# Kernel optimization log

Hardware: AMD Instinct MI355X
Metric: run time of the kernel (lower is better)

## Reference

```python
import jax, jax.numpy as jnp
import numpy as np

LAYERS = 3
EMB = 256
B = 4096
N_ITEMS = 50000
MAX_LEN = 50
EPS = 1e-12  # F.normalize eps


def setup_inputs() -> dict:
    key = jax.random.key(0)
    k1, k2, k3, k4, k5, k6 = jax.random.split(key, 6)
    item_embedding = jax.random.normal(k1, (N_ITEMS, EMB), dtype=jnp.float32)
    D = jax.random.uniform(k2, (B, B), dtype=jnp.float32)
    A = jax.random.uniform(k3, (B, B), dtype=jnp.float32)
    # indices into padded table of size N_ITEMS+1 (row 0 is the zero pad row)
    session_item = jax.random.randint(k4, (B, MAX_LEN), 0, N_ITEMS + 1, dtype=jnp.int64)
    session_len = jax.random.randint(k5, (B, 1), 1, MAX_LEN + 1).astype(jnp.float32)
    w_sess = jax.random.normal(k6, (LAYERS, EMB, EMB), dtype=jnp.float32) * (1.0 / np.sqrt(EMB))
    return {"item_embedding": item_embedding, "D": D, "A": A,
            "session_item": session_item, "session_len": session_len,
            "w_sess": w_sess}


def reference(item_embedding, D, A, session_item, session_len, w_sess):
    # prepend zero pad row, then gather: [B, L, E]
    emb = jnp.concatenate([jnp.zeros((1, item_embedding.shape[1]), item_embedding.dtype),
                           item_embedding], axis=0)
    seq_h = emb[session_item]                      # fused gather (no host round-trip)
    session_emb = seq_h.sum(axis=1) / session_len  # [B, E] mean pooling

    DA = D @ A                                     # [B, B]
    acc = session_emb                              # layer-0 (unnormalized) term
    x = session_emb
    for i in range(LAYERS):
        x = x @ w_sess[i].T                        # torch Linear: y = x W^T
        x = DA @ x                                 # dense GCN propagation
        norm = jnp.maximum(jnp.linalg.norm(x, axis=-1, keepdims=True), EPS)
        acc = acc + x / norm                       # normalized copy stored; x stays raw
    return acc / (LAYERS + 1)
```

## Files before the change

kernel.cpp:

```cpp
#include <hip/hip_runtime.h>
#include <hip/hip_bf16.h>
#include <cstdint>
#include <cstddef>

#define LAYERS 3
#define EMB 256
#define NB 4096
#define MAXLEN 50
#define NITEMS 50000

typedef float f32x4 __attribute__((ext_vector_type(4)));
typedef __bf16 bf16x8 __attribute__((ext_vector_type(8)));
typedef unsigned short u16;
typedef __attribute__((ext_vector_type(8))) unsigned short u16x8;

static __device__ __forceinline__ u16 f2bf(float f) {
  union { float f; uint32_t u; } v; v.f = f;
  uint32_t r = v.u + 0x7FFFu + ((v.u >> 16) & 1u);
  return (u16)(r >> 16);
}

static __device__ __forceinline__ float bf2f(u16 h) {
  union { uint32_t u; float f; } v; v.u = (uint32_t)h << 16; return v.f;
}

static __device__ __forceinline__ f32x4 bfu4(ushort4 h) {
  f32x4 r; r.x = bf2f(h.x); r.y = bf2f(h.y); r.z = bf2f(h.z); r.w = bf2f(h.w);
  return r;
}

static __device__ __forceinline__ ushort4 f2bf4(f32x4 v) {
  ushort4 o; o.x = f2bf(v.x); o.y = f2bf(v.y); o.z = f2bf(v.z); o.w = f2bf(v.w);
  return o;
}

template <typename T> __device__ __forceinline__ T cvt_out(float v);
template <> __device__ __forceinline__ float cvt_out<float>(float v) { return v; }
template <> __device__ __forceinline__ u16 cvt_out<u16>(float v) { return f2bf(v); }

#define N8_D (NB * NB / 8)
#define N8_W (LAYERS * EMB * EMB / 8)
#define N8_E ((NITEMS + 1) * EMB / 8)

__global__ void pack_all(const float* __restrict__ D, const float* __restrict__ A,
                         const float* __restrict__ w, const float* __restrict__ emb,
                         u16* __restrict__ Db, u16* __restrict__ Ab,
                         u16* __restrict__ wb, u16* __restrict__ ebp) {
  const int total = N8_D + N8_D + N8_W + N8_E;
  for (int i = blockIdx.x * blockDim.x + threadIdx.x; i < total;
       i += gridDim.x * blockDim.x) {
    int j = i;
    const float* src; u16* dst;
    if (j < N8_D) {
      src = D + (size_t)j * 8; dst = Db + (size_t)j * 8;
    } else if ((j -= N8_D) < N8_D) {
      src = A + (size_t)j * 8; dst = Ab + (size_t)j * 8;
    } else if ((j -= N8_D) < N8_W) {
      src = w + (size_t)j * 8; dst = wb + (size_t)j * 8;
    } else {
      j -= N8_W;
      dst = ebp + (size_t)j * 8;
      if (j < EMB / 8) {
        u16x8 z = {0, 0, 0, 0, 0, 0, 0, 0};
        *reinterpret_cast<u16x8*>(dst) = z;
        continue;
      }
      src = emb + (size_t)(j - EMB / 8) * 8;
    }
    f32x4 lo = *reinterpret_cast<const f32x4*>(src);
    f32x4 hi = *reinterpret_cast<const f32x4*>(src + 4);
    ushort4 a = f2bf4(lo), b = f2bf4(hi);
    u16x8 o = {a.x, a.y, a.z, a.w, b.x, b.y, b.z, b.w};
    *reinterpret_cast<u16x8*>(dst) = o;
  }
}

__global__ void gather_mean(const u16* __restrict__ ebp, const int* __restrict__ items,
                            const float* __restrict__ slen, float* __restrict__ acc,
                            u16* __restrict__ xb) {
  int w = threadIdx.x >> 6, lane = threadIdx.x & 63;
  int b = blockIdx.x * 4 + w;
  f32x4 s = {0.f, 0.f, 0.f, 0.f};
  const int* it = items + (size_t)b * MAXLEN;
  const int le = lane * 4;
#pragma unroll 2
  for (int l = 0; l < MAXLEN; l += 5) {
    int i0 = it[l], i1 = it[l + 1], i2 = it[l + 2], i3 = it[l + 3], i4 = it[l + 4];
    ushort4 v0 = *reinterpret_cast<const ushort4*>(ebp + (size_t)i0 * EMB + le);
    ushort4 v1 = *reinterpret_cast<const ushort4*>(ebp + (size_t)i1 * EMB + le);
    ushort4 v2 = *reinterpret_cast<const ushort4*>(ebp + (size_t)i2 * EMB + le);
    ushort4 v3 = *reinterpret_cast<const ushort4*>(ebp + (size_t)i3 * EMB + le);
    ushort4 v4 = *reinterpret_cast<const ushort4*>(ebp + (size_t)i4 * EMB + le);
    s += bfu4(v0) + bfu4(v1) + bfu4(v2) + bfu4(v3) + bfu4(v4);
  }
  float inv = 1.0f / slen[b];
  s *= inv;
  *reinterpret_cast<f32x4*>(acc + (size_t)b * EMB + le) = s;
  *reinterpret_cast<ushort4*>(xb + (size_t)b * EMB + le) = f2bf4(s);
}

template <int WR, int WC, typename OUT_T>
__global__ __launch_bounds__(512, 4) void gemm_w(const u16* __restrict__ Am,
                                                 const u16* __restrict__ Bt,
                                                 OUT_T* __restrict__ C,
                                                 int M, int N, int K, size_t zstride) {
  constexpr int TM = WR * 64, TN = WC * 64;
  __shared__ __align__(16) u16 As[TM * 64];
  __shared__ __align__(16) u16 Bs[TN * 64];
  const int tid = threadIdx.x;
  const int lane = tid & 63;
  const int wid = tid >> 6;
  const int wm = wid / WC, wn = wid % WC;
  const int row0 = blockIdx.y * TM, col0 = blockIdx.x * TN;
  const int kslice = K / (int)gridDim.z;
  const int kb = blockIdx.z * kslice, ke = kb + kslice;
  C += (size_t)blockIdx.z * zstride;

  f32x4 acc[4][4];
#pragma unroll
  for (int m = 0; m < 4; m++)
#pragma unroll
    for (int n = 0; n < 4; n++)
#pragma unroll
      for (int j = 0; j < 4; j++) acc[m][n][j] = 0.0f;

  const int lrow = lane & 15;
  const int lhi = lane >> 4;
  const int sw7 = lane & 7;
  const int srow = tid >> 3;
  const int schk = tid & 7;

  for (int k0 = kb; k0 < ke; k0 += 64) {
#pragma unroll
    for (int i = 0; i < WR; i++) {
      int row = i * 64 + srow;
      int sc = schk ^ (row & 7);
      __builtin_amdgcn_global_load_lds(
          (const __attribute__((address_space(1))) void*)(Am + (size_t)(row0 + row) * K + k0 + sc * 8),
          (__attribute__((address_space(3))) void*)(As + (size_t)(i * 512 + tid) * 8), 16, 0, 0);
    }
#pragma unroll
    for (int i = 0; i < WC; i++) {
      int row = i * 64 + srow;
      int sc = schk ^ (row & 7);
      __builtin_amdgcn_global_load_lds(
          (const __attribute__((address_space(1))) void*)(Bt + (size_t)(col0 + row) * K + k0 + sc * 8),
          (__attribute__((address_space(3))) void*)(Bs + (size_t)(i * 512 + tid) * 8), 16, 0, 0);
    }
    __syncthreads();

#pragma unroll
    for (int kk = 0; kk < 2; kk++) {
      const int co = ((kk * 4 + lhi) ^ sw7) * 8;
      bf16x8 af[4], bfv[4];
#pragma unroll
      for (int m = 0; m < 4; m++)
        af[m] = *reinterpret_cast<const bf16x8*>(As + (size_t)(wm * 64 + m * 16 + lrow) * 64 + co);
#pragma unroll
      for (int n = 0; n < 4; n++)
        bfv[n] = *reinterpret_cast<const bf16x8*>(Bs + (size_t)(wn * 64 + n * 16 + lrow) * 64 + co);
#pragma unroll
      for (int m = 0; m < 4; m++)
#pragma unroll
        for (int n = 0; n < 4; n++)
          acc[m][n] = __builtin_amdgcn_mfma_f32_16x16x32_bf16(af[m], bfv[n], acc[m][n], 0, 0, 0);
    }
    __syncthreads();
  }

#pragma unroll
  for (int m = 0; m < 4; m++) {
#pragma unroll
    for (int j = 0; j < 4; j++) {
      int r = row0 + wm * 64 + m * 16 + lhi * 4 + j;
      OUT_T* cp = C + (size_t)r * N + col0 + wn * 64 + lrow;
#pragma unroll
      for (int n = 0; n < 4; n++) cp[n * 16] = cvt_out<OUT_T>(acc[m][n][j]);
    }
  }
}

__global__ __launch_bounds__(256) void gemm64_ss(const u16* __restrict__ Am,
                                                 const u16* __restrict__ Bt,
                                                 u16* __restrict__ C, int N) {
  __shared__ __align__(16) u16 As[64 * 256];
  __shared__ __align__(16) u16 Bs[64 * 256];
  const int tid = threadIdx.x;
  const int lane = tid & 63;
  const int wid = tid >> 6;
  const int wr = wid >> 1, wc = wid & 1;
  const int row0 = blockIdx.y * 64, col0 = blockIdx.x * 64;
  const int lrow = lane & 15;
  const int lhi = lane >> 4;
  const int sw7 = lane & 7;

#pragma unroll
  for (int i = 0; i < 8; i++) {
    int row = i * 8 + (tid >> 5);
    int sc = (tid & 31) ^ (row & 7);
    __builtin_amdgcn_global_load_lds(
        (const __attribute__((address_space(1))) void*)(Am + (size_t)(row0 + row) * EMB + sc * 8),
        (__attribute__((address_space(3))) void*)((char*)As + (i * 256 + wid * 64) * 16), 16, 0, 0);
    __builtin_amdgcn_global_load_lds(
        (const __attribute__((address_space(1))) void*)(Bt + (size_t)(col0 + row) * EMB + sc * 8),
        (__attribute__((address_space(3))) void*)((char*)Bs + (i * 256 + wid * 64) * 16), 16, 0, 0);
  }
  __syncthreads();

  f32x4 acc[2][2];
#pragma unroll
  for (int m = 0; m < 2; m++)
#pragma unroll
    for (int n = 0; n < 2; n++)
#pragma unroll
      for (int j = 0; j < 4; j++) acc[m][n][j] = 0.0f;

#pragma unroll
  for (int ks = 0; ks < 8; ks++) {
    const int co = ((ks * 4 + lhi) ^ sw7) * 8;
    bf16x8 af[2], bfv[2];
#pragma unroll
    for (int m = 0; m < 2; m++)
      af[m] = *reinterpret_cast<const bf16x8*>(As + (size_t)(wr * 32 + m * 16 + lrow) * 256 + co);
#pragma unroll
    for (int n = 0; n < 2; n++)
      bfv[n] = *reinterpret_cast<const bf16x8*>(Bs + (size_t)(wc * 32 + n * 16 + lrow) * 256 + co);
#pragma unroll
    for (int m = 0; m < 2; m++)
#pragma unroll
      for (int n = 0; n < 2; n++)
        acc[m][n] = __builtin_amdgcn_mfma_f32_16x16x32_bf16(af[m], bfv[n], acc[m][n], 0, 0, 0);
  }

#pragma unroll
  for (int m = 0; m < 2; m++) {
#pragma unroll
    for (int j = 0; j < 4; j++) {
      int r = row0 + wr * 32 + m * 16 + lhi * 4 + j;
      u16* cp = C + (size_t)r * N + col0 + wc * 32 + lrow;
#pragma unroll
      for (int n = 0; n < 2; n++) cp[n * 16] = f2bf(acc[m][n][j]);
    }
  }
}

__global__ void uredux(const u16* __restrict__ zp, u16* __restrict__ uT,
                       int n4, int nsplit, size_t zstride4) {
  int i = blockIdx.x * blockDim.x + threadIdx.x;
  if (i < n4) {
    f32x4 s = {0.f, 0.f, 0.f, 0.f};
    for (int k = 0; k < nsplit; k++)
      s += bfu4(reinterpret_cast<const ushort4*>(zp)[(size_t)k * zstride4 + i]);
    reinterpret_cast<ushort4*>(uT)[i] = f2bf4(s);
  }
}

__global__ void norm_acc(const u16* __restrict__ zp, size_t zstride, int nsplit,
                         float* __restrict__ acc, u16* __restrict__ xb,
                         float* __restrict__ outp, int fin) {
  int b = blockIdx.x, t = threadIdx.x;
  size_t i = (size_t)b * EMB + t;
  float v = 0.0f;
  for (int s = 0; s < nsplit; s++) v += bf2f(zp[(size_t)s * zstride + i]);
  float s2 = v * v;
#pragma unroll
  for (int o = 32; o > 0; o >>= 1) s2 += __shfl_down(s2, o, 64);
  __shared__ float ws4[4];
  if ((t & 63) == 0) ws4[t >> 6] = s2;
  __syncthreads();
  float tot = ws4[0] + ws4[1] + ws4[2] + ws4[3];
  float rn = 1.0f / fmaxf(sqrtf(tot), 1e-12f);
  if (fin) {
    outp[i] = (acc[i] + v * rn) * 0.25f;
  } else {
    acc[i] += v * rn;
    xb[i] = f2bf(v);
  }
}

extern "C" void kernel_launch(void* const* d_in, const int* in_sizes, int n_in,
                              void* d_out, int out_size, void* d_ws, size_t ws_size,
                              hipStream_t stream) {
  const float* emb   = (const float*)d_in[0];
  const float* D     = (const float*)d_in[1];
  const float* A     = (const float*)d_in[2];
  const int*   items = (const int*)d_in[3];
  const float* slen  = (const float*)d_in[4];
  const float* w     = (const float*)d_in[5];
  float* out = (float*)d_out;

  char* p = (char*)d_ws;
  u16* Db   = (u16*)p;   p += (size_t)NB * NB * 2;
  u16* Ab   = (u16*)p;   p += (size_t)NB * NB * 2;
  float* accf = (float*)p; p += (size_t)NB * EMB * 4;
  u16* xb   = (u16*)p;   p += (size_t)NB * EMB * 2;
  u16* yT   = (u16*)p;   p += (size_t)EMB * NB * 2;
  u16* uT   = (u16*)p;   p += (size_t)EMB * NB * 2;
  u16* wb   = (u16*)p;   p += (size_t)LAYERS * EMB * EMB * 2;
  u16* ebp  = (u16*)p;   p += (size_t)(NITEMS + 1) * EMB * 2;
  u16* zp   = ebp;

  pack_all<<<2048, 256, 0, stream>>>(D, A, w, emb, Db, Ab, wb, ebp);
  gather_mean<<<NB / 4, 256, 0, stream>>>(ebp, items, slen, accf, xb);

  for (int i = 0; i < LAYERS; i++) {
    gemm64_ss<<<dim3(NB / 64, EMB / 64), 256, 0, stream>>>(wb + (size_t)i * EMB * EMB, xb, yT,
                                                           NB);
    gemm_w<4, 2, u16><<<dim3(NB / 128, 1, 8), 512, 0, stream>>>(
        yT, Ab, zp, EMB, NB, NB, (size_t)EMB * NB);
    uredux<<<EMB * NB / 4 / 256, 256, 0, stream>>>(zp, uT, EMB * NB / 4, 8,
                                                   (size_t)EMB * NB / 4);
    gemm_w<2, 4, u16><<<dim3(1, NB / 128, 8), 512, 0, stream>>>(
        Db, uT, zp, NB, EMB, NB, (size_t)NB * EMB);
    norm_acc<<<NB, 256, 0, stream>>>(zp, (size_t)NB * EMB, 8, accf, xb, out, i == LAYERS - 1);
  }
}
```

Baseline: 229.7 us.

## Gather fp32 embeddings directly and split packing into dedicated D/A and weight kernels

After: 237.3 us. +3.3%, slower.

```diff
diff --git a/kernel.cpp b/kernel.cpp
--- a/kernel.cpp
+++ b/kernel.cpp
@@ -12,7 +12,6 @@
 typedef float f32x4 __attribute__((ext_vector_type(4)));
 typedef __bf16 bf16x8 __attribute__((ext_vector_type(8)));
 typedef unsigned short u16;
-typedef __attribute__((ext_vector_type(8))) unsigned short u16x8;
 
 static __device__ __forceinline__ u16 f2bf(float f) {
   union { float f; uint32_t u; } v; v.f = f;
@@ -38,44 +37,32 @@
 template <> __device__ __forceinline__ float cvt_out<float>(float v) { return v; }
 template <> __device__ __forceinline__ u16 cvt_out<u16>(float v) { return f2bf(v); }
 
-#define N8_D (NB * NB / 8)
-#define N8_W (LAYERS * EMB * EMB / 8)
-#define N8_E ((NITEMS + 1) * EMB / 8)
-
-__global__ void pack_all(const float* __restrict__ D, const float* __restrict__ A,
-                         const float* __restrict__ w, const float* __restrict__ emb,
-                         u16* __restrict__ Db, u16* __restrict__ Ab,
-                         u16* __restrict__ wb, u16* __restrict__ ebp) {
-  const int total = N8_D + N8_D + N8_W + N8_E;
-  for (int i = blockIdx.x * blockDim.x + threadIdx.x; i < total;
-       i += gridDim.x * blockDim.x) {
-    int j = i;
-    const float* src; u16* dst;
-    if (j < N8_D) {
-      src = D + (size_t)j * 8; dst = Db + (size_t)j * 8;
-    } else if ((j -= N8_D) < N8_D) {
-      src = A + (size_t)j * 8; dst = Ab + (size_t)j * 8;
-    } else if ((j -= N8_D) < N8_W) {
-      src = w + (size_t)j * 8; dst = wb + (size_t)j * 8;
-    } else {
-      j -= N8_W;
-      dst = ebp + (size_t)j * 8;
-      if (j < EMB / 8) {
-        u16x8 z = {0, 0, 0, 0, 0, 0, 0, 0};
-        *reinterpret_cast<u16x8*>(dst) = z;
-        continue;
-      }
-      src = emb + (size_t)(j - EMB / 8) * 8;
-    }
-    f32x4 lo = *reinterpret_cast<const f32x4*>(src);
-    f32x4 hi = *reinterpret_cast<const f32x4*>(src + 4);
-    ushort4 a = f2bf4(lo), b = f2bf4(hi);
-    u16x8 o = {a.x, a.y, a.z, a.w, b.x, b.y, b.z, b.w};
-    *reinterpret_cast<u16x8*>(dst) = o;
-  }
-}
-
-__global__ void gather_mean(const u16* __restrict__ ebp, const int* __restrict__ items,
+#define N4_D (NB * NB / 4)
+
+__global__ void pack_pair(const float* __restrict__ D, const float* __restrict__ A,
+                          u16* __restrict__ Db, u16* __restrict__ Ab) {
+  const float* src = blockIdx.y ? A : D;
+  u16* dst = blockIdx.y ? Ab : Db;
+  const int stride = gridDim.x * blockDim.x;
+  const int i = blockIdx.x * blockDim.x + threadIdx.x;
+#pragma unroll 1
+  for (int o = 0; o < N4_D; o += 8 * stride) {
+    f32x4 v[8];
+#pragma unroll
+    for (int k = 0; k < 8; k++)
+      v[k] = reinterpret_cast<const f32x4*>(src)[o + i + k * stride];
+#pragma unroll
+    for (int k = 0; k < 8; k++)
+      reinterpret_cast<ushort4*>(dst)[o + i + k * stride] = f2bf4(v[k]);
+  }
+}
+
+__global__ void pack_w(const float* __restrict__ in, u16* __restrict__ out) {
+  int i = blockIdx.x * blockDim.x + threadIdx.x;
+  reinterpret_cast<ushort4*>(out)[i] = f2bf4(reinterpret_cast<const f32x4*>(in)[i]);
+}
+
+__global__ void gather_mean(const float* __restrict__ emb, const int* __restrict__ items,
                             const float* __restrict__ slen, float* __restrict__ acc,
                             u16* __restrict__ xb) {
   int w = threadIdx.x >> 6, lane = threadIdx.x & 63;
@@ -86,12 +73,13 @@
 #pragma unroll 2
   for (int l = 0; l < MAXLEN; l += 5) {
     int i0 = it[l], i1 = it[l + 1], i2 = it[l + 2], i3 = it[l + 3], i4 = it[l + 4];
-    ushort4 v0 = *reinterpret_cast<const ushort4*>(ebp + (size_t)i0 * EMB + le);
-    ushort4 v1 = *reinterpret_cast<const ushort4*>(ebp + (size_t)i1 * EMB + le);
-    ushort4 v2 = *reinterpret_cast<const ushort4*>(ebp + (size_t)i2 * EMB + le);
-    ushort4 v3 = *reinterpret_cast<const ushort4*>(ebp + (size_t)i3 * EMB + le);
-    ushort4 v4 = *reinterpret_cast<const ushort4*>(ebp + (size_t)i4 * EMB + le);
-    s += bfu4(v0) + bfu4(v1) + bfu4(v2) + bfu4(v3) + bfu4(v4);
+    f32x4 v0 = *reinterpret_cast<const f32x4*>(emb + (size_t)(i0 > 0 ? i0 - 1 : 0) * EMB + le);
+    f32x4 v1 = *reinterpret_cast<const f32x4*>(emb + (size_t)(i1 > 0 ? i1 - 1 : 0) * EMB + le);
+    f32x4 v2 = *reinterpret_cast<const f32x4*>(emb + (size_t)(i2 > 0 ? i2 - 1 : 0) * EMB + le);
+    f32x4 v3 = *reinterpret_cast<const f32x4*>(emb + (size_t)(i3 > 0 ? i3 - 1 : 0) * EMB + le);
+    f32x4 v4 = *reinterpret_cast<const f32x4*>(emb + (size_t)(i4 > 0 ? i4 - 1 : 0) * EMB + le);
+    s += v0 * (i0 > 0 ? 1.f : 0.f) + v1 * (i1 > 0 ? 1.f : 0.f) + v2 * (i2 > 0 ? 1.f : 0.f) +
+         v3 * (i3 > 0 ? 1.f : 0.f) + v4 * (i4 > 0 ? 1.f : 0.f);
   }
   float inv = 1.0f / slen[b];
   s *= inv;
@@ -292,16 +280,16 @@
   char* p = (char*)d_ws;
   u16* Db   = (u16*)p;   p += (size_t)NB * NB * 2;
   u16* Ab   = (u16*)p;   p += (size_t)NB * NB * 2;
+  u16* zp   = (u16*)p;   p += (size_t)8 * NB * EMB * 2;
   float* accf = (float*)p; p += (size_t)NB * EMB * 4;
   u16* xb   = (u16*)p;   p += (size_t)NB * EMB * 2;
   u16* yT   = (u16*)p;   p += (size_t)EMB * NB * 2;
   u16* uT   = (u16*)p;   p += (size_t)EMB * NB * 2;
   u16* wb   = (u16*)p;   p += (size_t)LAYERS * EMB * EMB * 2;
-  u16* ebp  = (u16*)p;   p += (size_t)(NITEMS + 1) * EMB * 2;
-  u16* zp   = ebp;
-
-  pack_all<<<2048, 256, 0, stream>>>(D, A, w, emb, Db, Ab, wb, ebp);
-  gather_mean<<<NB / 4, 256, 0, stream>>>(ebp, items, slen, accf, xb);
+
+  pack_pair<<<dim3(1024, 2), 256, 0, stream>>>(D, A, Db, Ab);
+  pack_w<<<LAYERS * EMB * EMB / 4 / 256, 256, 0, stream>>>(w, wb);
+  gather_mean<<<NB / 4, 256, 0, stream>>>(emb, items, slen, accf, xb);
 
   for (int i = 0; i < LAYERS; i++) {
     gemm64_ss<<<dim3(NB / 64, EMB / 64), 256, 0, stream>>>(wb + (size_t)i * EMB * EMB, xb, yT,
```
